# Kernel optimization log

Hardware: AMD Instinct MI355X
Metric: run time of the kernel (lower is better)

## Reference

```python
import jax, jax.numpy as jnp
import numpy as np

N, M, D_IN, D_K = 2048, 1024, 128, 64


def setup_inputs() -> dict:
    key = jax.random.key(0)
    kq, kk, kw = jax.random.split(key, 3)
    q = jax.random.normal(kq, (N, D_IN), dtype=jnp.float32)
    k = jax.random.normal(kk, (M, D_IN), dtype=jnp.float32)
    # glorot-uniform init for the bias-free Linear(d_in -> d_k) weight [d_k, d_in]
    limit = np.sqrt(6.0 / (D_IN + D_K)).astype(np.float32)
    W = jax.random.uniform(kw, (D_K, D_IN), dtype=jnp.float32, minval=-limit, maxval=limit)
    return {"q": q, "k": k, "W": W}


def reference(q, k, W):
    # pairwise broadcast difference: [n, m, d_in]
    diff = q[:, None, :] - k[None, :, :]
    # linear projection (nn.Linear: x @ W.T): [n, m, d_k]
    proj = jnp.einsum("nmd,kd->nmk", diff, W)
    # L2 norm over last dim: [n, m]
    dist = jnp.sqrt(jnp.sum(proj * proj, axis=-1))
    score = -dist * 0.5
    # masked_softmax with mask=None over dim=-1 == plain softmax over m
    return jax.nn.softmax(score, axis=-1)
```

## Files before the change

kernel.cpp:

```cpp
#include <hip/hip_runtime.h>
#include <math.h>

#define N_Q 2048
#define M_K 1024
#define DIN 128
#define DK  64

__global__ __launch_bounds__(256) void proj_kernel(
    const float* __restrict__ q, const float* __restrict__ k,
    const float* __restrict__ W, float* __restrict__ Qp,
    float* __restrict__ KpT, float* __restrict__ qn2, float* __restrict__ kn2)
{
    __shared__ float W_lds[DK][DIN + 4];
    __shared__ float row_lds[4][DIN];
    const int tx = threadIdx.x;

    const float4* W4 = (const float4*)W;
    #pragma unroll
    for (int i = 0; i < 8; ++i) {
        int idx = tx + i * 256;
        float4 v = W4[idx];
        int r = idx >> 5, c = (idx & 31) * 4;
        *(float4*)&W_lds[r][c] = v;
    }

    const int wave = tx >> 6, lane = tx & 63;
    const int row  = blockIdx.x * 4 + wave;
    const float* src = (row < N_Q) ? (q + (size_t)row * DIN)
                                   : (k + (size_t)(row - N_Q) * DIN);
    row_lds[wave][lane]      = src[lane];
    row_lds[wave][lane + 64] = src[lane + 64];
    __syncthreads();

    float acc = 0.f;
    #pragma unroll
    for (int d = 0; d < DIN; d += 4) {
        float4 wv = *(const float4*)&W_lds[lane][d];
        float4 rv = *(const float4*)&row_lds[wave][d];
        acc = fmaf(wv.x, rv.x, acc);
        acc = fmaf(wv.y, rv.y, acc);
        acc = fmaf(wv.z, rv.z, acc);
        acc = fmaf(wv.w, rv.w, acc);
    }

    float sq = acc * acc;
    #pragma unroll
    for (int off = 32; off >= 1; off >>= 1)
        sq += __shfl_xor(sq, off, 64);

    if (row < N_Q) {
        Qp[(size_t)row * DK + lane] = acc;
        if (lane == 0) qn2[row] = sq;
    } else {
        const int m = row - N_Q;
        KpT[(size_t)lane * M_K + m] = acc;
        if (lane == 0) kn2[m] = sq;
    }
}

__global__ __launch_bounds__(1024) void score_kernel(
    const float* __restrict__ Qp, const float* __restrict__ KpT,
    const float* __restrict__ qn2, const float* __restrict__ kn2,
    float* __restrict__ out)
{
    __shared__ float qpT[DK][8];
    __shared__ float qn2s[8];
    __shared__ float redmax[8][4];
    __shared__ float redsum[8][4];

    const int tx = threadIdx.x;
    const int n0 = blockIdx.x * 8;
    const int rg = tx >> 8;
    const int cg = tx & 255;
    const int lane = tx & 63;
    const int wInRow = (tx >> 6) & 3;

    if (tx < 512) {
        int d = tx >> 3, r = tx & 7;
        qpT[d][r] = Qp[(size_t)(n0 + r) * DK + d];
    }
    if (tx < 8) qn2s[tx] = qn2[n0 + tx];
    __syncthreads();

    float acc[2][4];
    #pragma unroll
    for (int r = 0; r < 2; ++r)
        #pragma unroll
        for (int i = 0; i < 4; ++i) acc[r][i] = 0.f;

    const float4* K4 = (const float4*)KpT;
    #pragma unroll 4
    for (int d = 0; d < DK; ++d) {
        float4 kv = K4[d * (M_K / 4) + cg];
        float2 qv = *(const float2*)&qpT[d][rg * 2];
        float kvv[4] = {kv.x, kv.y, kv.z, kv.w};
        #pragma unroll
        for (int i = 0; i < 4; ++i) {
            acc[0][i] = fmaf(qv.x, kvv[i], acc[0][i]);
            acc[1][i] = fmaf(qv.y, kvv[i], acc[1][i]);
        }
    }

    float4 kv2 = ((const float4*)kn2)[cg];
    float kn2a[4] = {kv2.x, kv2.y, kv2.z, kv2.w};
    #pragma unroll
    for (int r = 0; r < 2; ++r) {
        float qn = qn2s[rg * 2 + r];
        #pragma unroll
        for (int i = 0; i < 4; ++i) {
            float d2 = fmaxf(fmaf(-2.f, acc[r][i], qn + kn2a[i]), 0.f);
            acc[r][i] = -0.5f * sqrtf(d2);
        }
    }

    #pragma unroll
    for (int r = 0; r < 2; ++r) {
        float m = fmaxf(fmaxf(acc[r][0], acc[r][1]), fmaxf(acc[r][2], acc[r][3]));
        #pragma unroll
        for (int off = 32; off >= 1; off >>= 1)
            m = fmaxf(m, __shfl_xor(m, off, 64));
        if (lane == 0) redmax[rg * 2 + r][wInRow] = m;
    }
    __syncthreads();

    float mx[2];
    #pragma unroll
    for (int r = 0; r < 2; ++r) {
        const float* rm = redmax[rg * 2 + r];
        mx[r] = fmaxf(fmaxf(rm[0], rm[1]), fmaxf(rm[2], rm[3]));
    }

    #pragma unroll
    for (int r = 0; r < 2; ++r) {
        float t = 0.f;
        #pragma unroll
        for (int i = 0; i < 4; ++i) {
            acc[r][i] = __expf(acc[r][i] - mx[r]);
            t += acc[r][i];
        }
        #pragma unroll
        for (int off = 32; off >= 1; off >>= 1)
            t += __shfl_xor(t, off, 64);
        if (lane == 0) redsum[rg * 2 + r][wInRow] = t;
    }
    __syncthreads();

    #pragma unroll
    for (int r = 0; r < 2; ++r) {
        const float* rs = redsum[rg * 2 + r];
        float inv = 1.0f / (rs[0] + rs[1] + rs[2] + rs[3]);
        float4 o = make_float4(acc[r][0] * inv, acc[r][1] * inv,
                               acc[r][2] * inv, acc[r][3] * inv);
        ((float4*)out)[(size_t)(n0 + rg * 2 + r) * (M_K / 4) + cg] = o;
    }
}

extern "C" void kernel_launch(void* const* d_in, const int* in_sizes, int n_in,
                              void* d_out, int out_size, void* d_ws, size_t ws_size,
                              hipStream_t stream)
{
    const float* q = (const float*)d_in[0];
    const float* k = (const float*)d_in[1];
    const float* W = (const float*)d_in[2];
    float* out = (float*)d_out;

    float* Qp  = (float*)d_ws;
    float* KpT = Qp + (size_t)N_Q * DK;
    float* qn2 = KpT + (size_t)DK * M_K;
    float* kn2 = qn2 + N_Q;

    proj_kernel<<<(N_Q + M_K) / 4, 256, 0, stream>>>(q, k, W, Qp, KpT, qn2, kn2);
    score_kernel<<<N_Q / 8, 1024, 0, stream>>>(Qp, KpT, qn2, kn2, out);
}
```

Measured before the change: 23.42 us.

## Use split-bf16 MFMA for Q·K dot products and batch projection rows

The projection kernel now handles 32 rows per block and writes each projected value as a bf16 high/low pair, with K stored row-major instead of transposed. The score kernel computes the Q·K inner products with 16x16x32 bf16 MFMA instructions, using three cross terms to approximate fp32 accuracy, and processes 16 query rows per block. This replaces the scalar fp32 FMA loop with matrix-core work. In exchange, the dropped low×low term and bf16 rounding reduce precision, and the output stores become scalar and strided instead of float4.

```diff
diff --git a/kernel.cpp b/kernel.cpp
--- a/kernel.cpp
+++ b/kernel.cpp
@@ -1,4 +1,5 @@
 #include <hip/hip_runtime.h>
+#include <hip/hip_bf16.h>
 #include <math.h>
 
 #define N_Q 2048
@@ -6,152 +7,187 @@
 #define DIN 128
 #define DK  64
 
-__global__ __launch_bounds__(256) void proj_kernel(
+typedef __attribute__((ext_vector_type(8))) short short8;
+typedef __attribute__((ext_vector_type(4))) float f32x4;
+
+__global__ __launch_bounds__(512) void proj_split_kernel(
     const float* __restrict__ q, const float* __restrict__ k,
-    const float* __restrict__ W, float* __restrict__ Qp,
-    float* __restrict__ KpT, float* __restrict__ qn2, float* __restrict__ kn2)
+    const float* __restrict__ W,
+    unsigned short* __restrict__ Qh, unsigned short* __restrict__ Ql,
+    unsigned short* __restrict__ Kh, unsigned short* __restrict__ Kl,
+    float* __restrict__ qn2, float* __restrict__ kn2)
 {
     __shared__ float W_lds[DK][DIN + 4];
-    __shared__ float row_lds[4][DIN];
+    __shared__ float row_lds[32][DIN];
     const int tx = threadIdx.x;
 
     const float4* W4 = (const float4*)W;
     #pragma unroll
-    for (int i = 0; i < 8; ++i) {
-        int idx = tx + i * 256;
+    for (int i = 0; i < 4; ++i) {
+        int idx = tx + i * 512;
         float4 v = W4[idx];
         int r = idx >> 5, c = (idx & 31) * 4;
         *(float4*)&W_lds[r][c] = v;
     }
 
+    const int R0 = blockIdx.x * 32;
+    const bool isQ = (R0 < N_Q);
+    const float* src = isQ ? (q + (size_t)R0 * DIN)
+                           : (k + (size_t)(R0 - N_Q) * DIN);
+    const float4* src4 = (const float4*)src;
+    #pragma unroll
+    for (int i = 0; i < 2; ++i) {
+        int idx = tx + i * 512;
+        float4 v = src4[idx];
+        int r = idx >> 5, c = (idx & 31) * 4;
+        *(float4*)&row_lds[r][c] = v;
+    }
+    __syncthreads();
+
     const int wave = tx >> 6, lane = tx & 63;
-    const int row  = blockIdx.x * 4 + wave;
-    const float* src = (row < N_Q) ? (q + (size_t)row * DIN)
-                                   : (k + (size_t)(row - N_Q) * DIN);
-    row_lds[wave][lane]      = src[lane];
-    row_lds[wave][lane + 64] = src[lane + 64];
-    __syncthreads();
-
-    float acc = 0.f;
+    float acc[4] = {0.f, 0.f, 0.f, 0.f};
     #pragma unroll
     for (int d = 0; d < DIN; d += 4) {
         float4 wv = *(const float4*)&W_lds[lane][d];
-        float4 rv = *(const float4*)&row_lds[wave][d];
-        acc = fmaf(wv.x, rv.x, acc);
-        acc = fmaf(wv.y, rv.y, acc);
-        acc = fmaf(wv.z, rv.z, acc);
-        acc = fmaf(wv.w, rv.w, acc);
-    }
-
-    float sq = acc * acc;
-    #pragma unroll
-    for (int off = 32; off >= 1; off >>= 1)
-        sq += __shfl_xor(sq, off, 64);
-
-    if (row < N_Q) {
-        Qp[(size_t)row * DK + lane] = acc;
-        if (lane == 0) qn2[row] = sq;
-    } else {
-        const int m = row - N_Q;
-        KpT[(size_t)lane * M_K + m] = acc;
-        if (lane == 0) kn2[m] = sq;
+        #pragma unroll
+        for (int r = 0; r < 4; ++r) {
+            float4 rv = *(const float4*)&row_lds[wave * 4 + r][d];
+            acc[r] = fmaf(wv.x, rv.x, acc[r]);
+            acc[r] = fmaf(wv.y, rv.y, acc[r]);
+            acc[r] = fmaf(wv.z, rv.z, acc[r]);
+            acc[r] = fmaf(wv.w, rv.w, acc[r]);
+        }
+    }
+
+    #pragma unroll
+    for (int r = 0; r < 4; ++r) {
+        const int row = R0 + wave * 4 + r;
+        const float v = acc[r];
+        __hip_bfloat16 hb = __float2bfloat16(v);
+        float hf = __bfloat162float(hb);
+        __hip_bfloat16 lb = __float2bfloat16(v - hf);
+        float sq = v * v;
+        #pragma unroll
+        for (int off = 32; off >= 1; off >>= 1)
+            sq += __shfl_xor(sq, off, 64);
+        if (isQ) {
+            Qh[(size_t)row * DK + lane] = *(unsigned short*)&hb;
+            Ql[(size_t)row * DK + lane] = *(unsigned short*)&lb;
+            if (lane == 0) qn2[row] = sq;
+        } else {
+            const int m = row - N_Q;
+            Kh[(size_t)m * DK + lane] = *(unsigned short*)&hb;
+            Kl[(size_t)m * DK + lane] = *(unsigned short*)&lb;
+            if (lane == 0) kn2[m] = sq;
+        }
     }
 }
 
-__global__ __launch_bounds__(1024) void score_kernel(
-    const float* __restrict__ Qp, const float* __restrict__ KpT,
+__global__ __launch_bounds__(512) void score_kernel(
+    const unsigned short* __restrict__ Qh, const unsigned short* __restrict__ Ql,
+    const unsigned short* __restrict__ Kh, const unsigned short* __restrict__ Kl,
     const float* __restrict__ qn2, const float* __restrict__ kn2,
     float* __restrict__ out)
 {
-    __shared__ float qpT[DK][8];
-    __shared__ float qn2s[8];
-    __shared__ float redmax[8][4];
-    __shared__ float redsum[8][4];
+    __shared__ float redmax[16][8];
+    __shared__ float redsum[16][8];
 
     const int tx = threadIdx.x;
-    const int n0 = blockIdx.x * 8;
-    const int rg = tx >> 8;
-    const int cg = tx & 255;
-    const int lane = tx & 63;
-    const int wInRow = (tx >> 6) & 3;
-
-    if (tx < 512) {
-        int d = tx >> 3, r = tx & 7;
-        qpT[d][r] = Qp[(size_t)(n0 + r) * DK + d];
-    }
-    if (tx < 8) qn2s[tx] = qn2[n0 + tx];
+    const int w = tx >> 6, l = tx & 63;
+    const int g = l >> 4, c = l & 15;
+    const int n0 = blockIdx.x * 16;
+
+    const unsigned short* qrh = Qh + (size_t)(n0 + c) * DK;
+    const unsigned short* qrl = Ql + (size_t)(n0 + c) * DK;
+    const short8 Ah0 = *(const short8*)(qrh + g * 8);
+    const short8 Ah1 = *(const short8*)(qrh + 32 + g * 8);
+    const short8 Al0 = *(const short8*)(qrl + g * 8);
+    const short8 Al1 = *(const short8*)(qrl + 32 + g * 8);
+
+    float qn[4];
+    #pragma unroll
+    for (int j = 0; j < 4; ++j) qn[j] = qn2[n0 + 4 * g + j];
+
+    float s[8][4];
+    #pragma unroll
+    for (int t = 0; t < 8; ++t) {
+        const int m = w * 128 + t * 16 + c;
+        const unsigned short* krh = Kh + (size_t)m * DK;
+        const unsigned short* krl = Kl + (size_t)m * DK;
+        short8 Bh0 = *(const short8*)(krh + g * 8);
+        short8 Bh1 = *(const short8*)(krh + 32 + g * 8);
+        short8 Bl0 = *(const short8*)(krl + g * 8);
+        short8 Bl1 = *(const short8*)(krl + 32 + g * 8);
+
+        f32x4 acc = {0.f, 0.f, 0.f, 0.f};
+        acc = __builtin_amdgcn_mfma_f32_16x16x32_bf16(Ah0, Bh0, acc, 0, 0, 0);
+        acc = __builtin_amdgcn_mfma_f32_16x16x32_bf16(Ah1, Bh1, acc, 0, 0, 0);
+        acc = __builtin_amdgcn_mfma_f32_16x16x32_bf16(Ah0, Bl0, acc, 0, 0, 0);
+        acc = __builtin_amdgcn_mfma_f32_16x16x32_bf16(Ah1, Bl1, acc, 0, 0, 0);
+        acc = __builtin_amdgcn_mfma_f32_16x16x32_bf16(Al0, Bh0, acc, 0, 0, 0);
+        acc = __builtin_amdgcn_mfma_f32_16x16x32_bf16(Al1, Bh1, acc, 0, 0, 0);
+
+        const float kn = kn2[m];
+        #pragma unroll
+        for (int j = 0; j < 4; ++j) {
+            float d2 = fmaxf(qn[j] + kn - 2.f * acc[j], 0.f);
+            s[t][j] = -0.5f * sqrtf(d2);
+        }
+    }
+
+    #pragma unroll
+    for (int j = 0; j < 4; ++j) {
+        float m8 = s[0][j];
+        #pragma unroll
+        for (int t = 1; t < 8; ++t) m8 = fmaxf(m8, s[t][j]);
+        m8 = fmaxf(m8, __shfl_xor(m8, 1, 64));
+        m8 = fmaxf(m8, __shfl_xor(m8, 2, 64));
+        m8 = fmaxf(m8, __shfl_xor(m8, 4, 64));
+        m8 = fmaxf(m8, __shfl_xor(m8, 8, 64));
+        if (c == 0) redmax[4 * g + j][w] = m8;
+    }
     __syncthreads();
 
-    float acc[2][4];
-    #pragma unroll
-    for (int r = 0; r < 2; ++r)
-        #pragma unroll
-        for (int i = 0; i < 4; ++i) acc[r][i] = 0.f;
-
-    const float4* K4 = (const float4*)KpT;
-    #pragma unroll 4
-    for (int d = 0; d < DK; ++d) {
-        float4 kv = K4[d * (M_K / 4) + cg];
-        float2 qv = *(const float2*)&qpT[d][rg * 2];
-        float kvv[4] = {kv.x, kv.y, kv.z, kv.w};
-        #pragma unroll
-        for (int i = 0; i < 4; ++i) {
-            acc[0][i] = fmaf(qv.x, kvv[i], acc[0][i]);
-            acc[1][i] = fmaf(qv.y, kvv[i], acc[1][i]);
-        }
-    }
-
-    float4 kv2 = ((const float4*)kn2)[cg];
-    float kn2a[4] = {kv2.x, kv2.y, kv2.z, kv2.w};
-    #pragma unroll
-    for (int r = 0; r < 2; ++r) {
-        float qn = qn2s[rg * 2 + r];
-        #pragma unroll
-        for (int i = 0; i < 4; ++i) {
-            float d2 = fmaxf(fmaf(-2.f, acc[r][i], qn + kn2a[i]), 0.f);
-            acc[r][i] = -0.5f * sqrtf(d2);
-        }
-    }
-
-    #pragma unroll
-    for (int r = 0; r < 2; ++r) {
-        float m = fmaxf(fmaxf(acc[r][0], acc[r][1]), fmaxf(acc[r][2], acc[r][3]));
-        #pragma unroll
-        for (int off = 32; off >= 1; off >>= 1)
-            m = fmaxf(m, __shfl_xor(m, off, 64));
-        if (lane == 0) redmax[rg * 2 + r][wInRow] = m;
+    float mx[4];
+    #pragma unroll
+    for (int j = 0; j < 4; ++j) {
+        float m = redmax[4 * g + j][0];
+        #pragma unroll
+        for (int ww = 1; ww < 8; ++ww) m = fmaxf(m, redmax[4 * g + j][ww]);
+        mx[j] = m;
+    }
+
+    #pragma unroll
+    for (int j = 0; j < 4; ++j) {
+        float t8 = 0.f;
+        #pragma unroll
+        for (int t = 0; t < 8; ++t) {
+            s[t][j] = __expf(s[t][j] - mx[j]);
+            t8 += s[t][j];
+        }
+        t8 += __shfl_xor(t8, 1, 64);
+        t8 += __shfl_xor(t8, 2, 64);
+        t8 += __shfl_xor(t8, 4, 64);
+        t8 += __shfl_xor(t8, 8, 64);
+        if (c == 0) redsum[4 * g + j][w] = t8;
     }
     __syncthreads();
 
-    float mx[2];
-    #pragma unroll
-    for (int r = 0; r < 2; ++r) {
-        const float* rm = redmax[rg * 2 + r];
-        mx[r] = fmaxf(fmaxf(rm[0], rm[1]), fmaxf(rm[2], rm[3]));
-    }
-
-    #pragma unroll
-    for (int r = 0; r < 2; ++r) {
+    float inv[4];
+    #pragma unroll
+    for (int j = 0; j < 4; ++j) {
         float t = 0.f;
         #pragma unroll
-        for (int i = 0; i < 4; ++i) {
-            acc[r][i] = __expf(acc[r][i] - mx[r]);
-            t += acc[r][i];
-        }
-        #pragma unroll
-        for (int off = 32; off >= 1; off >>= 1)
-            t += __shfl_xor(t, off, 64);
-        if (lane == 0) redsum[rg * 2 + r][wInRow] = t;
-    }
-    __syncthreads();
-
-    #pragma unroll
-    for (int r = 0; r < 2; ++r) {
-        const float* rs = redsum[rg * 2 + r];
-        float inv = 1.0f / (rs[0] + rs[1] + rs[2] + rs[3]);
-        float4 o = make_float4(acc[r][0] * inv, acc[r][1] * inv,
-                               acc[r][2] * inv, acc[r][3] * inv);
-        ((float4*)out)[(size_t)(n0 + rg * 2 + r) * (M_K / 4) + cg] = o;
+        for (int ww = 0; ww < 8; ++ww) t += redsum[4 * g + j][ww];
+        inv[j] = 1.0f / t;
+    }
+
+    #pragma unroll
+    for (int t = 0; t < 8; ++t) {
+        const int m = w * 128 + t * 16 + c;
+        #pragma unroll
+        for (int j = 0; j < 4; ++j)
+            out[(size_t)(n0 + 4 * g + j) * M_K + m] = s[t][j] * inv[j];
     }
 }
 
@@ -164,11 +200,16 @@
     const float* W = (const float*)d_in[2];
     float* out = (float*)d_out;
 
-    float* Qp  = (float*)d_ws;
-    float* KpT = Qp + (size_t)N_Q * DK;
-    float* qn2 = KpT + (size_t)DK * M_K;
-    float* kn2 = qn2 + N_Q;
-
-    proj_kernel<<<(N_Q + M_K) / 4, 256, 0, stream>>>(q, k, W, Qp, KpT, qn2, kn2);
-    score_kernel<<<N_Q / 8, 1024, 0, stream>>>(Qp, KpT, qn2, kn2, out);
+    unsigned char* base = (unsigned char*)d_ws;
+    unsigned short* Qh = (unsigned short*)(base);
+    unsigned short* Ql = (unsigned short*)(base + 262144);
+    unsigned short* Kh = (unsigned short*)(base + 524288);
+    unsigned short* Kl = (unsigned short*)(base + 655360);
+    float* qn2 = (float*)(base + 786432);
+    float* kn2 = (float*)(base + 794624);
+
+    proj_split_kernel<<<(N_Q + M_K) / 32, 512, 0, stream>>>(
+        q, k, W, Qh, Ql, Kh, Kl, qn2, kn2);
+    score_kernel<<<N_Q / 16, 512, 0, stream>>>(
+        Qh, Ql, Kh, Kl, qn2, kn2, out);
 }
```

Result: slower. 62.76 us (+168.0%).
